# Optimization experiments

Measured on AMD Instinct MI355X. Metric: run time of the kernel, lower is better.

The kernel has to match this reference:

```python
import jax, jax.numpy as jnp
import numpy as np

FEATURES = 2048
BATCH = 16384
N_PAIRS = FEATURES * (FEATURES - 1) // 2  # 2,096,128


def setup_inputs() -> dict:
    key = jax.random.key(0)
    k1, k2, k3, k4 = jax.random.split(key, 4)
    x = jax.random.normal(k1, (BATCH, FEATURES), dtype=jnp.float32)
    # original torch.rand initializers -> uniform [0, 1)
    w0 = jax.random.uniform(k2, (1, 1), dtype=jnp.float32)
    w = jax.random.uniform(k3, (FEATURES, 1), dtype=jnp.float32)
    bw = jax.random.uniform(k4, (N_PAIRS, 1), dtype=jnp.float32)
    return {"x": x, "w0": w0, "w": w, "bw": bw}


def reference(x, w0, w, bw):
    # Pairwise cross term: sum_{j1<j2} bw[i] * x[:, j1] * x[:, j2]
    # Loop order (j1 outer, j2 inner, j1 < j2) is exactly the row-major
    # strictly-upper-triangle order of jnp.triu_indices(k=1).
    F = x.shape[1]
    iu = jnp.triu_indices(F, k=1)
    B = jnp.zeros((F, F), dtype=x.dtype).at[iu].set(bw[:, 0])  # [F, F]
    cross = jnp.einsum('bi,ij,bj->b', x, B, x)[:, None]        # [batch, 1]
    logits = x @ w + w0 + cross                                 # [batch, 1]
    return jax.nn.sigmoid(logits)
```

## Files before the change

### kernel.cpp

```cpp
#include <hip/hip_runtime.h>
#include <hip/hip_bf16.h>

#define F 2048
#define MB 16384
#define BM 128
#define BN 128
#define BK 32
#define PLANE (BM * BK)

typedef short bf16x8 __attribute__((ext_vector_type(8)));
typedef float f32x4 __attribute__((ext_vector_type(4)));

static __device__ __forceinline__ unsigned short bfb(float v) {
    return __builtin_bit_cast(unsigned short, __float2bfloat16(v));
}
static __device__ __forceinline__ float bff(unsigned short u) {
    return __bfloat162float(__builtin_bit_cast(__hip_bfloat16, u));
}

__global__ __launch_bounds__(256) void build_bt(const float* __restrict__ bw,
                                                unsigned short* __restrict__ bt_hi,
                                                unsigned short* __restrict__ bt_lo) {
    int idx = blockIdx.x * 256 + threadIdx.x;
    int j2 = idx >> 11;
    int j1 = idx & (F - 1);
    float v = 0.f;
    if (j1 < j2) {
        int k = j1 * F - ((j1 * (j1 + 1)) >> 1) + (j2 - j1 - 1);
        v = bw[k];
    }
    unsigned short h = bfb(v);
    bt_hi[idx] = h;
    bt_lo[idx] = bfb(v - bff(h));
}

__global__ __launch_bounds__(256, 2) void poly2_gemm(
        const float* __restrict__ x,
        const unsigned short* __restrict__ bt_hi,
        const unsigned short* __restrict__ bt_lo,
        const float* __restrict__ w,
        float* __restrict__ cross_acc) {
    extern __shared__ unsigned short smem[];

    const int tid  = threadIdx.x;
    const int lane = tid & 63;
    const int wid  = tid >> 6;
    const int wm   = wid >> 1;
    const int wn   = wid & 1;
    const int lr   = lane & 15;
    const int lg   = lane >> 4;

    const int nt = 15 - (blockIdx.x >> 7);
    const int mt = blockIdx.x & 127;
    const int m0 = mt * BM;
    const int n0 = nt * BN;
    const int ktiles = 4 * (nt + 1);

    f32x4 acc[4][4] = {};

    auto stageB = [&](int buf, int k0) {
        unsigned short* Bh = smem + buf * 4 * PLANE + 2 * PLANE;
        unsigned short* Bl = Bh + PLANE;
#pragma unroll
        for (int r = 0; r < 2; ++r) {
            int q = r * 256 + tid;
            int c = q >> 2, s = q & 3;
            int d = s ^ (c & 3);
            const unsigned short* ghi = bt_hi + (size_t)(n0 + c) * F + (k0 + d * 8);
            const unsigned short* glo = bt_lo + (size_t)(n0 + c) * F + (k0 + d * 8);
            unsigned short* dh = Bh + (q & ~63) * 8;
            unsigned short* dl = Bl + (q & ~63) * 8;
            __builtin_amdgcn_global_load_lds(
                (const __attribute__((address_space(1))) unsigned int*)ghi,
                (__attribute__((address_space(3))) unsigned int*)dh, 16, 0, 0);
            __builtin_amdgcn_global_load_lds(
                (const __attribute__((address_space(1))) unsigned int*)glo,
                (__attribute__((address_space(3))) unsigned int*)dl, 16, 0, 0);
        }
    };
    auto loadA = [&](int k0, float4* av) {
#pragma unroll
        for (int r = 0; r < 2; ++r) {
            int q = r * 256 + tid;
            int row = q >> 2, d = q & 3;
            const float* src = x + (size_t)(m0 + row) * F + (k0 + d * 8);
            av[r * 2 + 0] = *(const float4*)(src);
            av[r * 2 + 1] = *(const float4*)(src + 4);
        }
    };
    auto writeA = [&](int buf, const float4* av) {
        unsigned short* Ah = smem + buf * 4 * PLANE;
        unsigned short* Al = Ah + PLANE;
#pragma unroll
        for (int r = 0; r < 2; ++r) {
            int q = r * 256 + tid;
            int row = q >> 2, d = q & 3, s = d ^ (row & 3);
            float vv[8] = {av[r*2].x, av[r*2].y, av[r*2].z, av[r*2].w,
                           av[r*2+1].x, av[r*2+1].y, av[r*2+1].z, av[r*2+1].w};
            unsigned hw[8], lw[8];
#pragma unroll
            for (int j = 0; j < 8; ++j) {
                unsigned short h = bfb(vv[j]);
                hw[j] = h;
                lw[j] = bfb(vv[j] - bff(h));
            }
            uint4 hp, lp;
            hp.x = hw[0] | (hw[1] << 16); hp.y = hw[2] | (hw[3] << 16);
            hp.z = hw[4] | (hw[5] << 16); hp.w = hw[6] | (hw[7] << 16);
            lp.x = lw[0] | (lw[1] << 16); lp.y = lw[2] | (lw[3] << 16);
            lp.z = lw[4] | (lw[5] << 16); lp.w = lw[6] | (lw[7] << 16);
            *(uint4*)&Ah[row * 32 + s * 8] = hp;
            *(uint4*)&Al[row * 32 + s * 8] = lp;
        }
    };

    {
        float4 av[4];
        stageB(0, 0);
        loadA(0, av);
        writeA(0, av);
    }
    __syncthreads();

    int cur = 0;
    for (int kt = 0; kt < ktiles; ++kt) {
        const bool more = (kt + 1) < ktiles;
        float4 av[4];
        if (more) {
            stageB(cur ^ 1, (kt + 1) * BK);
            loadA((kt + 1) * BK, av);
        }

        unsigned short* Ah = smem + cur * 4 * PLANE;
        unsigned short* Al = Ah + PLANE;
        unsigned short* Bh = Al + PLANE;
        unsigned short* Bl = Bh + PLANE;
        const int sl = lg ^ (lr & 3);
        bf16x8 ah[4], al[4], bh[4], bl[4];
#pragma unroll
        for (int m = 0; m < 4; ++m) {
            int row = wm * 64 + m * 16 + lr;
            ah[m] = *(const bf16x8*)&Ah[row * 32 + sl * 8];
            al[m] = *(const bf16x8*)&Al[row * 32 + sl * 8];
        }
#pragma unroll
        for (int n = 0; n < 4; ++n) {
            int c = wn * 64 + n * 16 + lr;
            bh[n] = *(const bf16x8*)&Bh[c * 32 + sl * 8];
            bl[n] = *(const bf16x8*)&Bl[c * 32 + sl * 8];
        }
#pragma unroll
        for (int m = 0; m < 4; ++m)
#pragma unroll
            for (int n = 0; n < 4; ++n) {
                acc[m][n] = __builtin_amdgcn_mfma_f32_16x16x32_bf16(ah[m], bh[n], acc[m][n], 0, 0, 0);
                acc[m][n] = __builtin_amdgcn_mfma_f32_16x16x32_bf16(ah[m], bl[n], acc[m][n], 0, 0, 0);
                acc[m][n] = __builtin_amdgcn_mfma_f32_16x16x32_bf16(al[m], bh[n], acc[m][n], 0, 0, 0);
            }

        if (more) writeA(cur ^ 1, av);
        __syncthreads();
        cur ^= 1;
    }

#pragma unroll
    for (int m = 0; m < 4; ++m) {
#pragma unroll
        for (int r = 0; r < 4; ++r) {
            int grow = m0 + wm * 64 + m * 16 + lg * 4 + r;
            float sum = 0.f;
#pragma unroll
            for (int n = 0; n < 4; ++n) {
                int gcol = n0 + wn * 64 + n * 16 + lr;
                float y = acc[m][n][r] + w[gcol];
                sum += y * x[(size_t)grow * F + gcol];
            }
            sum += __shfl_xor(sum, 1);
            sum += __shfl_xor(sum, 2);
            sum += __shfl_xor(sum, 4);
            sum += __shfl_xor(sum, 8);
            if (lr == 0) atomicAdd(&cross_acc[grow], sum);
        }
    }
}

__global__ __launch_bounds__(256) void finish_sigmoid(const float* __restrict__ cross,
                                                      const float* __restrict__ w0,
                                                      float* __restrict__ out) {
    int b = blockIdx.x * 256 + threadIdx.x;
    float z = cross[b] + w0[0];
    out[b] = 1.f / (1.f + expf(-z));
}

extern "C" void kernel_launch(void* const* d_in, const int* in_sizes, int n_in,
                              void* d_out, int out_size, void* d_ws, size_t ws_size,
                              hipStream_t stream) {
    const float* x  = (const float*)d_in[0];
    const float* w0 = (const float*)d_in[1];
    const float* w  = (const float*)d_in[2];
    const float* bw = (const float*)d_in[3];
    float* out = (float*)d_out;

    float* cross = (float*)d_ws;
    unsigned short* bt_hi = (unsigned short*)((char*)d_ws + (size_t)MB * sizeof(float));
    unsigned short* bt_lo = bt_hi + (size_t)F * F;

    hipMemsetAsync(cross, 0, (size_t)MB * sizeof(float), stream);
    build_bt<<<F * F / 256, 256, 0, stream>>>(bw, bt_hi, bt_lo);
    size_t smem = (size_t)(2 * 4 * PLANE) * sizeof(unsigned short);
    poly2_gemm<<<dim3((MB / BM) * (F / BN)), 256, smem, stream>>>(x, bt_hi, bt_lo, w, cross);
    finish_sigmoid<<<MB / 256, 256, 0, stream>>>(cross, w0, out);
}
```

Before: 464.0 us.

## Load B operand directly from global into registers and double BK

```diff
diff --git a/kernel.cpp b/kernel.cpp
--- a/kernel.cpp
+++ b/kernel.cpp
@@ -5,7 +5,7 @@
 #define MB 16384
 #define BM 128
 #define BN 128
-#define BK 32
+#define BK 64
 #define PLANE (BM * BK)
 
 typedef short bf16x8 __attribute__((ext_vector_type(8)));
@@ -54,47 +54,27 @@
     const int mt = blockIdx.x & 127;
     const int m0 = mt * BM;
     const int n0 = nt * BN;
-    const int ktiles = 4 * (nt + 1);
+    const int ktiles = 2 * (nt + 1);
 
     f32x4 acc[4][4] = {};
 
-    auto stageB = [&](int buf, int k0) {
-        unsigned short* Bh = smem + buf * 4 * PLANE + 2 * PLANE;
-        unsigned short* Bl = Bh + PLANE;
-#pragma unroll
-        for (int r = 0; r < 2; ++r) {
+    auto loadA = [&](int k0, float4* av) {
+#pragma unroll
+        for (int r = 0; r < 4; ++r) {
             int q = r * 256 + tid;
-            int c = q >> 2, s = q & 3;
-            int d = s ^ (c & 3);
-            const unsigned short* ghi = bt_hi + (size_t)(n0 + c) * F + (k0 + d * 8);
-            const unsigned short* glo = bt_lo + (size_t)(n0 + c) * F + (k0 + d * 8);
-            unsigned short* dh = Bh + (q & ~63) * 8;
-            unsigned short* dl = Bl + (q & ~63) * 8;
-            __builtin_amdgcn_global_load_lds(
-                (const __attribute__((address_space(1))) unsigned int*)ghi,
-                (__attribute__((address_space(3))) unsigned int*)dh, 16, 0, 0);
-            __builtin_amdgcn_global_load_lds(
-                (const __attribute__((address_space(1))) unsigned int*)glo,
-                (__attribute__((address_space(3))) unsigned int*)dl, 16, 0, 0);
-        }
-    };
-    auto loadA = [&](int k0, float4* av) {
-#pragma unroll
-        for (int r = 0; r < 2; ++r) {
-            int q = r * 256 + tid;
-            int row = q >> 2, d = q & 3;
+            int row = q >> 3;
+            int d = (q & 7) ^ (row & 7);
             const float* src = x + (size_t)(m0 + row) * F + (k0 + d * 8);
-            av[r * 2 + 0] = *(const float4*)(src);
-            av[r * 2 + 1] = *(const float4*)(src + 4);
+            av[r * 2 + 0] = ((const float4*)src)[0];
+            av[r * 2 + 1] = ((const float4*)src)[1];
         }
     };
     auto writeA = [&](int buf, const float4* av) {
-        unsigned short* Ah = smem + buf * 4 * PLANE;
+        unsigned short* Ah = smem + buf * 2 * PLANE;
         unsigned short* Al = Ah + PLANE;
 #pragma unroll
-        for (int r = 0; r < 2; ++r) {
+        for (int r = 0; r < 4; ++r) {
             int q = r * 256 + tid;
-            int row = q >> 2, d = q & 3, s = d ^ (row & 3);
             float vv[8] = {av[r*2].x, av[r*2].y, av[r*2].z, av[r*2].w,
                            av[r*2+1].x, av[r*2+1].y, av[r*2+1].z, av[r*2+1].w};
             unsigned hw[8], lw[8];
@@ -109,54 +89,78 @@
             hp.z = hw[4] | (hw[5] << 16); hp.w = hw[6] | (hw[7] << 16);
             lp.x = lw[0] | (lw[1] << 16); lp.y = lw[2] | (lw[3] << 16);
             lp.z = lw[4] | (lw[5] << 16); lp.w = lw[6] | (lw[7] << 16);
-            *(uint4*)&Ah[row * 32 + s * 8] = hp;
-            *(uint4*)&Al[row * 32 + s * 8] = lp;
+            *(uint4*)&Ah[q * 8] = hp;
+            *(uint4*)&Al[q * 8] = lp;
         }
     };
+    auto loadB = [&](int k, bf16x8* bh, bf16x8* bl) {
+#pragma unroll
+        for (int n = 0; n < 4; ++n) {
+            int c = n0 + wn * 64 + n * 16 + lr;
+            size_t off = (size_t)c * F + k + lg * 8;
+            bh[n] = *(const bf16x8*)(bt_hi + off);
+            bl[n] = *(const bf16x8*)(bt_lo + off);
+        }
+    };
+
+    bf16x8 b0h[4], b0l[4], b1h[4], b1l[4];
 
     {
-        float4 av[4];
-        stageB(0, 0);
+        float4 av[8];
         loadA(0, av);
         writeA(0, av);
+        loadB(0, b0h, b0l);
     }
     __syncthreads();
 
     int cur = 0;
     for (int kt = 0; kt < ktiles; ++kt) {
         const bool more = (kt + 1) < ktiles;
-        float4 av[4];
-        if (more) {
-            stageB(cur ^ 1, (kt + 1) * BK);
-            loadA((kt + 1) * BK, av);
-        }
-
-        unsigned short* Ah = smem + cur * 4 * PLANE;
+        unsigned short* Ah = smem + cur * 2 * PLANE;
         unsigned short* Al = Ah + PLANE;
-        unsigned short* Bh = Al + PLANE;
-        unsigned short* Bl = Bh + PLANE;
-        const int sl = lg ^ (lr & 3);
-        bf16x8 ah[4], al[4], bh[4], bl[4];
-#pragma unroll
-        for (int m = 0; m < 4; ++m) {
-            int row = wm * 64 + m * 16 + lr;
-            ah[m] = *(const bf16x8*)&Ah[row * 32 + sl * 8];
-            al[m] = *(const bf16x8*)&Al[row * 32 + sl * 8];
-        }
-#pragma unroll
-        for (int n = 0; n < 4; ++n) {
-            int c = wn * 64 + n * 16 + lr;
-            bh[n] = *(const bf16x8*)&Bh[c * 32 + sl * 8];
-            bl[n] = *(const bf16x8*)&Bl[c * 32 + sl * 8];
-        }
-#pragma unroll
-        for (int m = 0; m < 4; ++m)
-#pragma unroll
-            for (int n = 0; n < 4; ++n) {
-                acc[m][n] = __builtin_amdgcn_mfma_f32_16x16x32_bf16(ah[m], bh[n], acc[m][n], 0, 0, 0);
-                acc[m][n] = __builtin_amdgcn_mfma_f32_16x16x32_bf16(ah[m], bl[n], acc[m][n], 0, 0, 0);
-                acc[m][n] = __builtin_amdgcn_mfma_f32_16x16x32_bf16(al[m], bh[n], acc[m][n], 0, 0, 0);
-            }
+
+        float4 av[8];
+        if (more) loadA((kt + 1) * BK, av);
+
+        loadB(kt * BK + 32, b1h, b1l);
+        {
+            bf16x8 ah[4], al[4];
+#pragma unroll
+            for (int m = 0; m < 4; ++m) {
+                int row = wm * 64 + m * 16 + lr;
+                int s = lg ^ (lr & 7);
+                ah[m] = *(const bf16x8*)&Ah[row * 64 + s * 8];
+                al[m] = *(const bf16x8*)&Al[row * 64 + s * 8];
+            }
+#pragma unroll
+            for (int m = 0; m < 4; ++m)
+#pragma unroll
+                for (int n = 0; n < 4; ++n) {
+                    acc[m][n] = __builtin_amdgcn_mfma_f32_16x16x32_bf16(ah[m], b0h[n], acc[m][n], 0, 0, 0);
+                    acc[m][n] = __builtin_amdgcn_mfma_f32_16x16x32_bf16(ah[m], b0l[n], acc[m][n], 0, 0, 0);
+                    acc[m][n] = __builtin_amdgcn_mfma_f32_16x16x32_bf16(al[m], b0h[n], acc[m][n], 0, 0, 0);
+                }
+        }
+
+        if (more) loadB((kt + 1) * BK, b0h, b0l);
+        {
+            bf16x8 ah[4], al[4];
+#pragma unroll
+            for (int m = 0; m < 4; ++m) {
+                int row = wm * 64 + m * 16 + lr;
+                int s = (4 + lg) ^ (lr & 7);
+                ah[m] = *(const bf16x8*)&Ah[row * 64 + s * 8];
+                al[m] = *(const bf16x8*)&Al[row * 64 + s * 8];
+            }
+#pragma unroll
+            for (int m = 0; m < 4; ++m)
+#pragma unroll
+                for (int n = 0; n < 4; ++n) {
+                    acc[m][n] = __builtin_amdgcn_mfma_f32_16x16x32_bf16(ah[m], b1h[n], acc[m][n], 0, 0, 0);
+                    acc[m][n] = __builtin_amdgcn_mfma_f32_16x16x32_bf16(ah[m], b1l[n], acc[m][n], 0, 0, 0);
+                    acc[m][n] = __builtin_amdgcn_mfma_f32_16x16x32_bf16(al[m], b1h[n], acc[m][n], 0, 0, 0);
+                }
+        }
 
         if (more) writeA(cur ^ 1, av);
         __syncthreads();
@@ -207,7 +211,7 @@
 
     hipMemsetAsync(cross, 0, (size_t)MB * sizeof(float), stream);
     build_bt<<<F * F / 256, 256, 0, stream>>>(bw, bt_hi, bt_lo);
-    size_t smem = (size_t)(2 * 4 * PLANE) * sizeof(unsigned short);
+    size_t smem = (size_t)(2 * 2 * PLANE) * sizeof(unsigned short);
     poly2_gemm<<<dim3((MB / BM) * (F / BN)), 256, smem, stream>>>(x, bt_hi, bt_lo, w, cross);
     finish_sigmoid<<<MB / 256, 256, 0, stream>>>(cross, w0, out);
 }
```

Result: slower. 530.7 us (+14.4%).

## Enlarge GEMM tiles to 256x256, rework LDS swizzle and transpose B via shared memory

Applied to the files above, without the earlier changes.

```diff
diff --git a/kernel.cpp b/kernel.cpp
--- a/kernel.cpp
+++ b/kernel.cpp
@@ -2,11 +2,12 @@
 #include <hip/hip_bf16.h>
 
 #define F 2048
-#define MB 16384
-#define BM 128
-#define BN 128
+#define MBATCH 16384
+#define BM 256
+#define BN 256
 #define BK 32
-#define PLANE (BM * BK)
+#define PL (BM * BK)
+#define THREADS 512
 
 typedef short bf16x8 __attribute__((ext_vector_type(8)));
 typedef float f32x4 __attribute__((ext_vector_type(4)));
@@ -16,25 +17,64 @@
 }
 static __device__ __forceinline__ float bff(unsigned short u) {
     return __bfloat162float(__builtin_bit_cast(__hip_bfloat16, u));
+}
+static __device__ __forceinline__ unsigned pack_hi16(float a, float b) {
+    return __builtin_amdgcn_perm(__builtin_bit_cast(unsigned, b),
+                                 __builtin_bit_cast(unsigned, a), 0x07060302u);
+}
+static __device__ __forceinline__ float trunc_hi(float v) {
+    return __builtin_bit_cast(float, __builtin_bit_cast(unsigned, v) & 0xffff0000u);
+}
+static __device__ __forceinline__ unsigned cvtpk_bf16(float a, float b) {
+    unsigned r;
+    asm("v_cvt_pk_bf16_f32 %0, %1, %2" : "=v"(r) : "v"(a), "v"(b));
+    return r;
 }
 
 __global__ __launch_bounds__(256) void build_bt(const float* __restrict__ bw,
                                                 unsigned short* __restrict__ bt_hi,
                                                 unsigned short* __restrict__ bt_lo) {
-    int idx = blockIdx.x * 256 + threadIdx.x;
-    int j2 = idx >> 11;
-    int j1 = idx & (F - 1);
-    float v = 0.f;
-    if (j1 < j2) {
-        int k = j1 * F - ((j1 * (j1 + 1)) >> 1) + (j2 - j1 - 1);
-        v = bw[k];
-    }
-    unsigned short h = bfb(v);
-    bt_hi[idx] = h;
-    bt_lo[idx] = bfb(v - bff(h));
-}
-
-__global__ __launch_bounds__(256, 2) void poly2_gemm(
+    __shared__ unsigned short tH[64][72], tL[64][72];
+    const int bx = blockIdx.x & 31;
+    const int by = blockIdx.x >> 5;
+    const int r  = threadIdx.x >> 2;
+    const int cg = (threadIdx.x & 3) * 16;
+    const bool up = (by >= bx);
+    if (up) {
+        int j1 = bx * 64 + r;
+        long base = (long)j1 * F - (((long)j1 * (j1 + 1)) >> 1) - j1 - 1;
+#pragma unroll
+        for (int c = 0; c < 16; ++c) {
+            int j2 = by * 64 + cg + c;
+            float v = (j2 > j1) ? bw[base + j2] : 0.f;
+            unsigned short h = bfb(v);
+            tH[r][cg + c] = h;
+            tL[r][cg + c] = bfb(v - bff(h));
+        }
+    }
+    __syncthreads();
+    size_t obase = (size_t)(by * 64 + r) * F + bx * 64 + cg;
+    uint4 H0 = {0,0,0,0}, H1 = {0,0,0,0}, L0 = {0,0,0,0}, L1 = {0,0,0,0};
+    if (up) {
+        unsigned oh[16], ol[16];
+#pragma unroll
+        for (int c = 0; c < 16; ++c) { oh[c] = tH[cg + c][r]; ol[c] = tL[cg + c][r]; }
+        H0.x = oh[0] | (oh[1] << 16);  H0.y = oh[2] | (oh[3] << 16);
+        H0.z = oh[4] | (oh[5] << 16);  H0.w = oh[6] | (oh[7] << 16);
+        H1.x = oh[8] | (oh[9] << 16);  H1.y = oh[10] | (oh[11] << 16);
+        H1.z = oh[12] | (oh[13] << 16); H1.w = oh[14] | (oh[15] << 16);
+        L0.x = ol[0] | (ol[1] << 16);  L0.y = ol[2] | (ol[3] << 16);
+        L0.z = ol[4] | (ol[5] << 16);  L0.w = ol[6] | (ol[7] << 16);
+        L1.x = ol[8] | (ol[9] << 16);  L1.y = ol[10] | (ol[11] << 16);
+        L1.z = ol[12] | (ol[13] << 16); L1.w = ol[14] | (ol[15] << 16);
+    }
+    *(uint4*)(bt_hi + obase)     = H0;
+    *(uint4*)(bt_hi + obase + 8) = H1;
+    *(uint4*)(bt_lo + obase)     = L0;
+    *(uint4*)(bt_lo + obase + 8) = L1;
+}
+
+__global__ __launch_bounds__(THREADS, 2) void poly2_gemm(
         const float* __restrict__ x,
         const unsigned short* __restrict__ bt_hi,
         const unsigned short* __restrict__ bt_lo,
@@ -45,29 +85,32 @@
     const int tid  = threadIdx.x;
     const int lane = tid & 63;
     const int wid  = tid >> 6;
-    const int wm   = wid >> 1;
-    const int wn   = wid & 1;
+    const int wm   = wid >> 2;
+    const int wn   = wid & 3;
     const int lr   = lane & 15;
     const int lg   = lane >> 4;
 
-    const int nt = 15 - (blockIdx.x >> 7);
-    const int mt = blockIdx.x & 127;
+    const int g  = blockIdx.x >> 6;
+    const int nt = (g < 4) ? (7 - g) : (g - 4);
+    const int mt = blockIdx.x & 63;
     const int m0 = mt * BM;
     const int n0 = nt * BN;
-    const int ktiles = 4 * (nt + 1);
-
-    f32x4 acc[4][4] = {};
+    const int ktiles = 8 * (nt + 1);
+
+    f32x4 acc[8][4] = {};
 
     auto stageB = [&](int buf, int k0) {
-        unsigned short* Bh = smem + buf * 4 * PLANE + 2 * PLANE;
-        unsigned short* Bl = Bh + PLANE;
-#pragma unroll
-        for (int r = 0; r < 2; ++r) {
-            int q = r * 256 + tid;
-            int c = q >> 2, s = q & 3;
-            int d = s ^ (c & 3);
-            const unsigned short* ghi = bt_hi + (size_t)(n0 + c) * F + (k0 + d * 8);
-            const unsigned short* glo = bt_lo + (size_t)(n0 + c) * F + (k0 + d * 8);
+        unsigned short* Bh = smem + buf * 4 * PL + 2 * PL;
+        unsigned short* Bl = Bh + PL;
+#pragma unroll
+        for (int it = 0; it < 2; ++it) {
+            int q  = it * THREADS + tid;
+            int rp = q >> 3, s = q & 7;
+            int h  = s ^ (rp & 7);
+            int col  = n0 + 2 * rp + (h >> 2);
+            int koff = k0 + (h & 3) * 8;
+            const unsigned short* ghi = bt_hi + (size_t)col * F + koff;
+            const unsigned short* glo = bt_lo + (size_t)col * F + koff;
             unsigned short* dh = Bh + (q & ~63) * 8;
             unsigned short* dl = Bl + (q & ~63) * 8;
             __builtin_amdgcn_global_load_lds(
@@ -78,102 +121,107 @@
                 (__attribute__((address_space(3))) unsigned int*)dl, 16, 0, 0);
         }
     };
-    auto loadA = [&](int k0, float4* av) {
-#pragma unroll
-        for (int r = 0; r < 2; ++r) {
-            int q = r * 256 + tid;
-            int row = q >> 2, d = q & 3;
-            const float* src = x + (size_t)(m0 + row) * F + (k0 + d * 8);
-            av[r * 2 + 0] = *(const float4*)(src);
-            av[r * 2 + 1] = *(const float4*)(src + 4);
-        }
-    };
-    auto writeA = [&](int buf, const float4* av) {
-        unsigned short* Ah = smem + buf * 4 * PLANE;
-        unsigned short* Al = Ah + PLANE;
-#pragma unroll
-        for (int r = 0; r < 2; ++r) {
-            int q = r * 256 + tid;
-            int row = q >> 2, d = q & 3, s = d ^ (row & 3);
-            float vv[8] = {av[r*2].x, av[r*2].y, av[r*2].z, av[r*2].w,
-                           av[r*2+1].x, av[r*2+1].y, av[r*2+1].z, av[r*2+1].w};
-            unsigned hw[8], lw[8];
-#pragma unroll
-            for (int j = 0; j < 8; ++j) {
-                unsigned short h = bfb(vv[j]);
-                hw[j] = h;
-                lw[j] = bfb(vv[j] - bff(h));
+    auto loadA = [&](int k0, float4* raw) {
+#pragma unroll
+        for (int hf = 0; hf < 2; ++hf) {
+            int q  = hf * THREADS + tid;
+            int rp = q >> 3, s = q & 7;
+            int h  = s ^ (rp & 7);
+            const float* src = x + (size_t)(m0 + 2 * rp + (h >> 2)) * F + k0 + (h & 3) * 8;
+            raw[hf * 2 + 0] = ((const float4*)src)[0];
+            raw[hf * 2 + 1] = ((const float4*)src)[1];
+        }
+    };
+    auto writeA = [&](int buf, const float4* raw) {
+        unsigned short* Ah = smem + buf * 4 * PL;
+        unsigned short* Al = Ah + PL;
+#pragma unroll
+        for (int hf = 0; hf < 2; ++hf) {
+            int q = hf * THREADS + tid;
+            float e0 = raw[hf*2].x, e1 = raw[hf*2].y, e2 = raw[hf*2].z, e3 = raw[hf*2].w;
+            float e4 = raw[hf*2+1].x, e5 = raw[hf*2+1].y, e6 = raw[hf*2+1].z, e7 = raw[hf*2+1].w;
+            uint4 H, L;
+            H.x = pack_hi16(e0, e1); H.y = pack_hi16(e2, e3);
+            H.z = pack_hi16(e4, e5); H.w = pack_hi16(e6, e7);
+            L.x = cvtpk_bf16(e0 - trunc_hi(e0), e1 - trunc_hi(e1));
+            L.y = cvtpk_bf16(e2 - trunc_hi(e2), e3 - trunc_hi(e3));
+            L.z = cvtpk_bf16(e4 - trunc_hi(e4), e5 - trunc_hi(e5));
+            L.w = cvtpk_bf16(e6 - trunc_hi(e6), e7 - trunc_hi(e7));
+            *(uint4*)&Ah[q * 8] = H;
+            *(uint4*)&Al[q * 8] = L;
+        }
+    };
+    auto compute = [&](int buf) {
+        const unsigned short* Ah = smem + buf * 4 * PL;
+        const unsigned short* Al = Ah + PL;
+        const unsigned short* Bh = Al + PL;
+        const unsigned short* Bl = Bh + PL;
+        bf16x8 bh[4], bl[4];
+#pragma unroll
+        for (int n = 0; n < 4; ++n) {
+            int c  = wn * 64 + n * 16 + lr;
+            int rp = c >> 1;
+            int off = rp * 64 + ((((c & 1) << 2) + lg) ^ (rp & 7)) * 8;
+            bh[n] = *(const bf16x8*)&Bh[off];
+            bl[n] = *(const bf16x8*)&Bl[off];
+        }
+#pragma unroll
+        for (int mh = 0; mh < 2; ++mh) {
+            bf16x8 ah[4], al[4];
+#pragma unroll
+            for (int m2 = 0; m2 < 4; ++m2) {
+                int r  = wm * 128 + (mh * 4 + m2) * 16 + lr;
+                int rp = r >> 1;
+                int off = rp * 64 + ((((r & 1) << 2) + lg) ^ (rp & 7)) * 8;
+                ah[m2] = *(const bf16x8*)&Ah[off];
+                al[m2] = *(const bf16x8*)&Al[off];
             }
-            uint4 hp, lp;
-            hp.x = hw[0] | (hw[1] << 16); hp.y = hw[2] | (hw[3] << 16);
-            hp.z = hw[4] | (hw[5] << 16); hp.w = hw[6] | (hw[7] << 16);
-            lp.x = lw[0] | (lw[1] << 16); lp.y = lw[2] | (lw[3] << 16);
-            lp.z = lw[4] | (lw[5] << 16); lp.w = lw[6] | (lw[7] << 16);
-            *(uint4*)&Ah[row * 32 + s * 8] = hp;
-            *(uint4*)&Al[row * 32 + s * 8] = lp;
+#pragma unroll
+            for (int m2 = 0; m2 < 4; ++m2)
+#pragma unroll
+                for (int n = 0; n < 4; ++n) {
+                    f32x4 c0 = acc[mh * 4 + m2][n];
+                    c0 = __builtin_amdgcn_mfma_f32_16x16x32_bf16(ah[m2], bh[n], c0, 0, 0, 0);
+                    c0 = __builtin_amdgcn_mfma_f32_16x16x32_bf16(ah[m2], bl[n], c0, 0, 0, 0);
+                    c0 = __builtin_amdgcn_mfma_f32_16x16x32_bf16(al[m2], bh[n], c0, 0, 0, 0);
+                    acc[mh * 4 + m2][n] = c0;
+                }
         }
     };
 
     {
-        float4 av[4];
+        float4 raw[4];
         stageB(0, 0);
-        loadA(0, av);
-        writeA(0, av);
+        loadA(0, raw);
+        writeA(0, raw);
     }
     __syncthreads();
 
     int cur = 0;
     for (int kt = 0; kt < ktiles; ++kt) {
         const bool more = (kt + 1) < ktiles;
-        float4 av[4];
+        float4 raw[4];
         if (more) {
             stageB(cur ^ 1, (kt + 1) * BK);
-            loadA((kt + 1) * BK, av);
-        }
-
-        unsigned short* Ah = smem + cur * 4 * PLANE;
-        unsigned short* Al = Ah + PLANE;
-        unsigned short* Bh = Al + PLANE;
-        unsigned short* Bl = Bh + PLANE;
-        const int sl = lg ^ (lr & 3);
-        bf16x8 ah[4], al[4], bh[4], bl[4];
-#pragma unroll
-        for (int m = 0; m < 4; ++m) {
-            int row = wm * 64 + m * 16 + lr;
-            ah[m] = *(const bf16x8*)&Ah[row * 32 + sl * 8];
-            al[m] = *(const bf16x8*)&Al[row * 32 + sl * 8];
-        }
-#pragma unroll
-        for (int n = 0; n < 4; ++n) {
-            int c = wn * 64 + n * 16 + lr;
-            bh[n] = *(const bf16x8*)&Bh[c * 32 + sl * 8];
-            bl[n] = *(const bf16x8*)&Bl[c * 32 + sl * 8];
-        }
-#pragma unroll
-        for (int m = 0; m < 4; ++m)
-#pragma unroll
-            for (int n = 0; n < 4; ++n) {
-                acc[m][n] = __builtin_amdgcn_mfma_f32_16x16x32_bf16(ah[m], bh[n], acc[m][n], 0, 0, 0);
-                acc[m][n] = __builtin_amdgcn_mfma_f32_16x16x32_bf16(ah[m], bl[n], acc[m][n], 0, 0, 0);
-                acc[m][n] = __builtin_amdgcn_mfma_f32_16x16x32_bf16(al[m], bh[n], acc[m][n], 0, 0, 0);
-            }
-
-        if (more) writeA(cur ^ 1, av);
+            loadA((kt + 1) * BK, raw);
+        }
+        compute(cur);
+        if (more) writeA(cur ^ 1, raw);
         __syncthreads();
         cur ^= 1;
     }
 
 #pragma unroll
-    for (int m = 0; m < 4; ++m) {
+    for (int m = 0; m < 8; ++m) {
 #pragma unroll
         for (int r = 0; r < 4; ++r) {
-            int grow = m0 + wm * 64 + m * 16 + lg * 4 + r;
+            int grow = m0 + wm * 128 + m * 16 + lg * 4 + r;
             float sum = 0.f;
 #pragma unroll
             for (int n = 0; n < 4; ++n) {
                 int gcol = n0 + wn * 64 + n * 16 + lr;
-                float y = acc[m][n][r] + w[gcol];
-                sum += y * x[(size_t)grow * F + gcol];
+                float yv = acc[m][n][r] + w[gcol];
+                sum += yv * x[(size_t)grow * F + gcol];
             }
             sum += __shfl_xor(sum, 1);
             sum += __shfl_xor(sum, 2);
@@ -202,12 +250,14 @@
     float* out = (float*)d_out;
 
     float* cross = (float*)d_ws;
-    unsigned short* bt_hi = (unsigned short*)((char*)d_ws + (size_t)MB * sizeof(float));
+    unsigned short* bt_hi = (unsigned short*)((char*)d_ws + (size_t)MBATCH * sizeof(float));
     unsigned short* bt_lo = bt_hi + (size_t)F * F;
 
-    hipMemsetAsync(cross, 0, (size_t)MB * sizeof(float), stream);
-    build_bt<<<F * F / 256, 256, 0, stream>>>(bw, bt_hi, bt_lo);
-    size_t smem = (size_t)(2 * 4 * PLANE) * sizeof(unsigned short);
-    poly2_gemm<<<dim3((MB / BM) * (F / BN)), 256, smem, stream>>>(x, bt_hi, bt_lo, w, cross);
-    finish_sigmoid<<<MB / 256, 256, 0, stream>>>(cross, w0, out);
-}
+    hipFuncSetAttribute((const void*)poly2_gemm,
+                        hipFuncAttributeMaxDynamicSharedMemorySize, 131072);
+
+    hipMemsetAsync(cross, 0, (size_t)MBATCH * sizeof(float), stream);
+    build_bt<<<(F / 64) * (F / 64), 256, 0, stream>>>(bw, bt_hi, bt_lo);
+    poly2_gemm<<<(MBATCH / BM) * (F / BN), THREADS, 131072, stream>>>(x, bt_hi, bt_lo, w, cross);
+    finish_sigmoid<<<MBATCH / 256, 256, 0, stream>>>(cross, w0, out);
+}
```

New measurement: 392.6 us. -15.4%, faster.
